# Performance work log

Hardware: AMD Instinct MI355X
Metric: run time of the kernel (lower is better)

Reference implementation:

```python
import jax, jax.numpy as jnp
import numpy as np

B, C_IN, V_IN = 16, 16, 16000
V1, V2 = 16384, 4096          # V2 = V1 // 4 (after first pool)
K1, K2 = 16, 16               # Chebyshev orders
F1, F2 = 32, 64               # conv output channels
FC1_F = 512
DEG = 16
EPS = 1e-5


def setup_inputs() -> dict:
    key = jax.random.key(0)
    ks = jax.random.split(key, 12)
    x = jax.random.normal(ks[0], (B, C_IN, V_IN), dtype=jnp.float32)
    perm_idx = jax.random.permutation(ks[1], V1).astype(jnp.int32)
    # sparse rescaled Laplacians in COO form (row, col, val)
    l1_rows = jnp.repeat(jnp.arange(V1, dtype=jnp.int32), DEG)
    l1_cols = jax.random.randint(ks[2], (V1 * DEG,), 0, V1, dtype=jnp.int32)
    l1_vals = jax.random.normal(ks[3], (V1 * DEG,), dtype=jnp.float32) / DEG
    l2_rows = jnp.repeat(jnp.arange(V2, dtype=jnp.int32), DEG)
    l2_cols = jax.random.randint(ks[4], (V2 * DEG,), 0, V2, dtype=jnp.int32)
    l2_vals = jax.random.normal(ks[5], (V2 * DEG,), dtype=jnp.float32) / DEG
    # Graph_Conv kernels: Linear(in_channels*K -> out_channels)
    s1 = np.sqrt(2.0 / (C_IN * K1 + F1)).astype(np.float32)
    w1 = jax.random.uniform(ks[6], (F1, C_IN * K1), jnp.float32, -s1, s1)
    b1 = jnp.zeros((F1,), jnp.float32)
    s2 = np.sqrt(2.0 / (F1 * K2 + F2)).astype(np.float32)
    w2 = jax.random.uniform(ks[7], (F2, F1 * K2), jnp.float32, -s2, s2)
    b2 = jnp.zeros((F2,), jnp.float32)
    fc_in = F2 * (V1 // 16)  # 65536
    s3 = np.sqrt(2.0 / (fc_in + FC1_F)).astype(np.float32)
    fc1_w = jax.random.uniform(ks[8], (FC1_F, fc_in), jnp.float32, -s3, s3)
    fc1_b = jnp.zeros((FC1_F,), jnp.float32)
    return dict(x=x, perm_idx=perm_idx,
                l1_rows=l1_rows, l1_cols=l1_cols, l1_vals=l1_vals,
                l2_rows=l2_rows, l2_cols=l2_cols, l2_vals=l2_vals,
                w1=w1, b1=b1, w2=w2, b2=b2, fc1_w=fc1_w, fc1_b=fc1_b)


def _spmm(rows, cols, vals, X, V):
    # sparse (V,V) @ dense (V,M) via gather + segment-sum
    return jax.ops.segment_sum(vals[:, None] * X[cols], rows, num_segments=V)


def _cheb_conv(x, rows, cols, vals, w, b, K):
    # x: (B, C, V) -> (B, Fout, V)
    Bn, C, V = x.shape
    x0 = x.transpose(2, 1, 0).reshape(V, C * Bn)
    xs = [x0]
    if K > 1:
        xs.append(_spmm(rows, cols, vals, x0, V))
    for _ in range(2, K):
        xs.append(2.0 * _spmm(rows, cols, vals, xs[-1], V) - xs[-2])
    xk = jnp.stack(xs, axis=0).reshape(K, V, C, Bn)    # (K, V, C, B)
    xk = xk.transpose(3, 1, 2, 0).reshape(Bn * V, C * K)
    y = xk @ w.T + b                                   # (B*V, Fout)
    return y.reshape(Bn, V, -1).transpose(0, 2, 1)     # (B, Fout, V)


def _pool4(x):
    Bn, C, V = x.shape
    return x.reshape(Bn, C, V // 4, 4).max(axis=-1)


def reference(x, perm_idx, l1_rows, l1_cols, l1_vals,
              l2_rows, l2_cols, l2_vals,
              w1, b1, w2, b2, fc1_w, fc1_b):
    # BatchNorm1d(affine=False), training-mode (batch) statistics
    mean = x.mean(axis=(0, 2), keepdims=True)
    var = x.var(axis=(0, 2), keepdims=True)
    x = (x - mean) * jax.lax.rsqrt(var + EPS)
    # Permute: zero-pad vertices to V1, then reorder
    Bn, C, V = x.shape
    x = jnp.pad(x, ((0, 0), (0, 0), (0, V1 - V)))[:, :, perm_idx]
    # conv1 -> relu -> pool4
    x = jax.nn.relu(_cheb_conv(x, l1_rows, l1_cols, l1_vals, w1, b1, K1))
    x = _pool4(x)
    # conv2 -> relu -> pool4
    x = jax.nn.relu(_cheb_conv(x, l2_rows, l2_cols, l2_vals, w2, b2, K2))
    x = _pool4(x)
    # flatten + fc1 (dropout is identity in eval mode)
    x = x.reshape(Bn, -1)
    return x @ fc1_w.T + fc1_b
```

## Files before the change

### kernel.cpp

```cpp
#include <hip/hip_runtime.h>

#define VIN  16000
#define V1q  16384
#define V2q  4096
#define Kq   16
#define F1q  32
#define F2q  64
#define FCIN 65536

typedef unsigned short u16;
typedef __attribute__((ext_vector_type(8))) short short8;
typedef __attribute__((ext_vector_type(4))) float f32x4;

__device__ __forceinline__ float bf2f(u16 v) { return __uint_as_float((unsigned)v << 16); }
__device__ __forceinline__ u16 f2bf(float f) {
    unsigned u = __float_as_uint(f);
    return (u16)((u + 0x7fffu + ((u >> 16) & 1u)) >> 16);
}

__global__ void bn_part(const float* __restrict__ x, float* __restrict__ part) {
    int c  = blockIdx.y;
    int bx = blockIdx.x;
    int b  = bx >> 2;
    int vc = bx & 3;
    const float* p = x + (size_t)(b * 16 + c) * VIN + vc * 4000;
    float s = 0.f, s2 = 0.f;
    for (int v = threadIdx.x; v < 4000; v += 256) {
        float val = p[v];
        s += val; s2 += val * val;
    }
    for (int o = 32; o; o >>= 1) { s += __shfl_down(s, o); s2 += __shfl_down(s2, o); }
    __shared__ float ls[4], ls2[4];
    int wid = threadIdx.x >> 6;
    if ((threadIdx.x & 63) == 0) { ls[wid] = s; ls2[wid] = s2; }
    __syncthreads();
    if (threadIdx.x == 0) {
        s = ls[0] + ls[1] + ls[2] + ls[3];
        s2 = ls2[0] + ls2[1] + ls2[2] + ls2[3];
        part[(c * 64 + bx) * 2]     = s;
        part[(c * 64 + bx) * 2 + 1] = s2;
    }
}

__global__ void bn_final(const float* __restrict__ part, float* __restrict__ mean_rstd) {
    int t = threadIdx.x;
    int c = t >> 4, j = t & 15;
    float s = 0.f, s2 = 0.f;
    for (int i = 0; i < 4; i++) {
        s  += part[(c * 64 + j * 4 + i) * 2];
        s2 += part[(c * 64 + j * 4 + i) * 2 + 1];
    }
    for (int o = 8; o; o >>= 1) { s += __shfl_down(s, o, 16); s2 += __shfl_down(s2, o, 16); }
    if (j == 0) {
        float m  = s / 256000.f;
        float var = s2 / 256000.f - m * m;
        mean_rstd[c]      = m;
        mean_rstd[16 + c] = rsqrtf(var + 1e-5f);
    }
}

__global__ void build_iperm(const int* __restrict__ perm, int* __restrict__ iperm) {
    int v = blockIdx.x * 256 + threadIdx.x;
    if (v < V1q) iperm[perm[v]] = v;
}

__global__ void norm_transpose_scatter(const float* __restrict__ x,
                                       const float* __restrict__ mean_rstd,
                                       const int* __restrict__ iperm,
                                       u16* __restrict__ X0) {
    __shared__ u16 tile[256][33];
    int u0 = blockIdx.x * 32;
    int t  = threadIdx.x;
    int jj = t & 31, half = t >> 5;
    for (int rr = 0; rr < 32; rr++) {
        int s = rr * 8 + half;
        int c = s & 15, b = s >> 4;
        float val = x[(size_t)s * VIN + u0 + jj];
        val = (val - mean_rstd[c]) * mean_rstd[16 + c];
        int d = ((c >> 3) << 7) | (b << 3) | (c & 7);
        tile[d][jj] = f2bf(val);
    }
    __syncthreads();
    for (int j = 0; j < 32; j++) {
        int tv = iperm[u0 + j];
        X0[(size_t)tv * 256 + t] = tile[t][j];
    }
}

__global__ void pack_w1(const float* __restrict__ w1, u16* __restrict__ B1p) {
    int i = blockIdx.x * 256 + threadIdx.x;
    int j = i & 7, l = (i >> 3) & 63, nf = (i >> 9) & 1, s = i >> 10;
    int q = l >> 4;
    int k = s * 2 + (q >> 1);
    int c = (q & 1) * 8 + j;
    int f = nf * 16 + (l & 15);
    B1p[i] = f2bf(w1[f * 256 + c * 16 + k]);
}
__global__ void pack_w2(const float* __restrict__ w2, u16* __restrict__ B2p) {
    int i = blockIdx.x * 256 + threadIdx.x;
    int j = i & 7, l = (i >> 3) & 63, nf = (i >> 9) & 3, k = i >> 11;
    int f1 = (l >> 4) * 8 + j;
    int f2 = nf * 16 + (l & 15);
    B2p[i] = f2bf(w2[f2 * 512 + f1 * 16 + k]);
}

template<int WLOG, int NRBLOG>
__global__ void spmm_cheb(const u16* __restrict__ prev, const u16* __restrict__ prev2,
                          u16* __restrict__ out,
                          const int* __restrict__ cols, const float* __restrict__ vals,
                          int nwg, float scale, int sub) {
    int bid = blockIdx.x;
    int q = nwg >> 3;
    int wid = (bid & 7) * q + (bid >> 3);
    int cb = wid >> NRBLOG;
    int r4 = wid & ((1 << NRBLOG) - 1);
    int lane = threadIdx.x & 63;
    int r = __builtin_amdgcn_readfirstlane(r4 * 4 + (threadIdx.x >> 6));
    int col = (cb << 6) + lane;
    const int4*   cp = (const int4*)(cols + r * 16);
    const float4* vp = (const float4*)(vals + r * 16);
    float acc = 0.f;
#pragma unroll
    for (int ii = 0; ii < 4; ii++) {
        int4   ci = cp[ii];
        float4 vi = vp[ii];
        const u16* p0 = prev + ((size_t)__builtin_amdgcn_readfirstlane(ci.x) << WLOG);
        const u16* p1 = prev + ((size_t)__builtin_amdgcn_readfirstlane(ci.y) << WLOG);
        const u16* p2 = prev + ((size_t)__builtin_amdgcn_readfirstlane(ci.z) << WLOG);
        const u16* p3 = prev + ((size_t)__builtin_amdgcn_readfirstlane(ci.w) << WLOG);
        acc += vi.x * bf2f(p0[col]);
        acc += vi.y * bf2f(p1[col]);
        acc += vi.z * bf2f(p2[col]);
        acc += vi.w * bf2f(p3[col]);
    }
    float o = scale * acc;
    if (sub) o -= bf2f(prev2[((size_t)r << WLOG) + col]);
    out[((size_t)r << WLOG) + col] = f2bf(o);
}

__launch_bounds__(256)
__global__ void gemm1_mfma(const u16* __restrict__ XS1, const u16* __restrict__ B1p,
                           const float* __restrict__ b1, u16* __restrict__ XS2_0) {
    __shared__ u16 As[2][4096];
    int t = threadIdx.x;
    int w = t >> 6, l = t & 63;
    int v0 = blockIdx.x * 8;
    int nf = w & 1, vq = w >> 1;

    f32x4 acc[4] = {};
    {
        const short8* s0 = (const short8*)(XS1 + (size_t)(0 * V1q + v0) * 256);
        const short8* s1 = (const short8*)(XS1 + (size_t)(1 * V1q + v0) * 256);
        short8* dst = (short8*)As[0];
        dst[t] = s0[t]; dst[256 + t] = s1[t];
    }
    __syncthreads();
    for (int s = 0; s < 8; s++) {
        int cur = s & 1;
        if (s < 7) {
            const short8* s0 = (const short8*)(XS1 + (size_t)((2 * s + 2) * V1q + v0) * 256);
            const short8* s1 = (const short8*)(XS1 + (size_t)((2 * s + 3) * V1q + v0) * 256);
            short8* dst = (short8*)As[cur ^ 1];
            dst[t] = s0[t]; dst[256 + t] = s1[t];
        }
        short8 bfrag = *(const short8*)(B1p + (((size_t)s * 2 + nf) * 64 + l) * 8);
        int abase = (l >> 5) * 2048 + (l & 31) * 8;
#pragma unroll
        for (int fm = 0; fm < 4; fm++) {
            int vl = vq * 4 + fm;
            short8 afrag = *(const short8*)&As[cur][abase + vl * 256];
            acc[fm] = __builtin_amdgcn_mfma_f32_16x16x32_bf16(afrag, bfrag, acc[fm], 0, 0, 0);
        }
        __syncthreads();
    }
    f32x4 m = acc[0];
#pragma unroll
    for (int fm = 1; fm < 4; fm++) {
#pragma unroll
        for (int i = 0; i < 4; i++) m[i] = fmaxf(m[i], acc[fm][i]);
    }
    int f1 = nf * 16 + (l & 15);
    float bias = b1[f1];
    int u_out = blockIdx.x * 2 + vq;
    u16* orow = XS2_0 + (size_t)u_out * 512;
    int colbase = ((f1 >> 3) << 7) | (f1 & 7);
#pragma unroll
    for (int reg = 0; reg < 4; reg++) {
        int b = (l >> 4) * 4 + reg;
        orow[colbase + b * 8] = f2bf(fmaxf(m[reg] + bias, 0.f));
    }
}

__launch_bounds__(256)
__global__ void gemm2_mfma(const u16* __restrict__ XS2, const u16* __restrict__ B2p,
                           const float* __restrict__ b2, float* __restrict__ P2f) {
    __shared__ u16 As[2][8192];
    __shared__ float ylds[4 * 16 * 66];
    int t = threadIdx.x;
    int w = t >> 6, l = t & 63;
    int u0 = blockIdx.x * 16;

    f32x4 acc[4][4] = {};
    {
        const short8* src = (const short8*)(XS2 + (size_t)(0 * V2q + u0) * 512);
        short8* dst = (short8*)As[0];
#pragma unroll
        for (int r = 0; r < 4; r++) dst[t * 4 + r] = src[t * 4 + r];
    }
    __syncthreads();
    for (int k = 0; k < 16; k++) {
        int cur = k & 1;
        if (k < 15) {
            const short8* src = (const short8*)(XS2 + (size_t)((k + 1) * V2q + u0) * 512);
            short8* dst = (short8*)As[cur ^ 1];
#pragma unroll
            for (int r = 0; r < 4; r++) dst[t * 4 + r] = src[t * 4 + r];
        }
        short8 bfrag[4];
#pragma unroll
        for (int nf = 0; nf < 4; nf++)
            bfrag[nf] = *(const short8*)(B2p + (((size_t)k * 4 + nf) * 64 + l) * 8);
#pragma unroll
        for (int fm = 0; fm < 4; fm++) {
            int ul = w * 4 + fm;
            short8 afrag = *(const short8*)&As[cur][ul * 512 + l * 8];
#pragma unroll
            for (int nf = 0; nf < 4; nf++)
                acc[fm][nf] = __builtin_amdgcn_mfma_f32_16x16x32_bf16(afrag, bfrag[nf], acc[fm][nf], 0, 0, 0);
        }
        __syncthreads();
    }
#pragma unroll
    for (int nf = 0; nf < 4; nf++) {
        int f2 = nf * 16 + (l & 15);
        float bias = b2[f2];
#pragma unroll
        for (int reg = 0; reg < 4; reg++) {
            int b = (l >> 4) * 4 + reg;
            float m = fmaxf(fmaxf(acc[0][nf][reg], acc[1][nf][reg]),
                            fmaxf(acc[2][nf][reg], acc[3][nf][reg]));
            ylds[(w * 16 + b) * 66 + f2] = fmaxf(m + bias, 0.f);
        }
    }
    __syncthreads();
    int ub = blockIdx.x * 4;
#pragma unroll
    for (int i = 0; i < 4; i++) {
        int p = t + i * 256;
        int b = p >> 6, f2 = p & 63;
        float4 v;
        v.x = ylds[(0 * 16 + b) * 66 + f2];
        v.y = ylds[(1 * 16 + b) * 66 + f2];
        v.z = ylds[(2 * 16 + b) * 66 + f2];
        v.w = ylds[(3 * 16 + b) * 66 + f2];
        *(float4*)&P2f[(size_t)(b * 64 + f2) * 1024 + ub] = v;
    }
}

__global__ void fc_init(const float* __restrict__ b, float* __restrict__ out) {
    int i = blockIdx.x * 256 + threadIdx.x;
    out[i] = b[i & 511];
}

__launch_bounds__(256)
__global__ void fc1k(const float* __restrict__ P2f, const float* __restrict__ W,
                     float* __restrict__ out) {
    __shared__ float red[4][64][17];
    int t = threadIdx.x;
    int w = t >> 6, l = t & 63;
    int o0 = blockIdx.x * 8 + w * 2;
    int k0 = blockIdx.y * 4096;
    const float* wr0 = W + (size_t)o0 * FCIN + k0;
    const float* wr1 = W + (size_t)(o0 + 1) * FCIN + k0;
    const float* pb  = P2f + k0;
    float acc0[16], acc1[16];
#pragma unroll
    for (int b = 0; b < 16; b++) { acc0[b] = 0.f; acc1[b] = 0.f; }
    for (int it = 0; it < 16; it++) {
        int kk = it * 256 + l * 4;
        float4 wa = *(const float4*)(wr0 + kk);
        float4 wb = *(const float4*)(wr1 + kk);
#pragma unroll
        for (int b = 0; b < 16; b++) {
            float4 p = *(const float4*)(pb + (size_t)b * FCIN + kk);
            acc0[b] += wa.x * p.x + wa.y * p.y + wa.z * p.z + wa.w * p.w;
            acc1[b] += wb.x * p.x + wb.y * p.y + wb.z * p.z + wb.w * p.w;
        }
    }
    int qq = l >> 4, bb = l & 15;
    __syncthreads();
#pragma unroll
    for (int b = 0; b < 16; b++) red[w][l][b] = acc0[b];
    __syncthreads();
    {
        float s = 0.f;
#pragma unroll
        for (int i = 0; i < 16; i++) s += red[w][qq * 16 + i][bb];
        s += __shfl_down(s, 16);
        s += __shfl_down(s, 32);
        if (l < 16) atomicAdd(&out[bb * 512 + o0], s);
    }
    __syncthreads();
#pragma unroll
    for (int b = 0; b < 16; b++) red[w][l][b] = acc1[b];
    __syncthreads();
    {
        float s = 0.f;
#pragma unroll
        for (int i = 0; i < 16; i++) s += red[w][qq * 16 + i][bb];
        s += __shfl_down(s, 16);
        s += __shfl_down(s, 32);
        if (l < 16) atomicAdd(&out[bb * 512 + o0 + 1], s);
    }
}

extern "C" void kernel_launch(void* const* d_in, const int* in_sizes, int n_in,
                              void* d_out, int out_size, void* d_ws, size_t ws_size,
                              hipStream_t stream) {
    const float* x       = (const float*)d_in[0];
    const int*   perm    = (const int*)d_in[1];
    const int*   l1_cols = (const int*)d_in[3];
    const float* l1_vals = (const float*)d_in[4];
    const int*   l2_cols = (const int*)d_in[6];
    const float* l2_vals = (const float*)d_in[7];
    const float* w1      = (const float*)d_in[8];
    const float* b1      = (const float*)d_in[9];
    const float* w2      = (const float*)d_in[10];
    const float* b2      = (const float*)d_in[11];
    const float* fcw     = (const float*)d_in[12];
    const float* fcb     = (const float*)d_in[13];
    float* out = (float*)d_out;

    char* wsb = (char*)d_ws;
    size_t off = 0;
    auto alloc = [&](size_t bytes) -> void* {
        void* p = wsb + off;
        off += (bytes + 255) & ~(size_t)255;
        return p;
    };
    float* mean_rstd = (float*)alloc(32 * 4);
    float* bnpart    = (float*)alloc(16 * 64 * 2 * 4);
    int*   iperm     = (int*)alloc((size_t)V1q * 4);
    u16*   B1p       = (u16*)alloc(8192 * 2);
    u16*   B2p       = (u16*)alloc(32768 * 2);
    u16*   XS1       = (u16*)alloc((size_t)Kq * V1q * 256 * 2);
    u16*   XS2       = (u16*)alloc((size_t)Kq * V2q * 512 * 2);
    float* P2f       = (float*)alloc((size_t)16 * FCIN * 4);
    (void)ws_size; (void)in_sizes; (void)n_in; (void)out_size;

    const size_t S1 = (size_t)V1q * 256;
    const size_t S2 = (size_t)V2q * 512;

    bn_part<<<dim3(64, 16), 256, 0, stream>>>(x, bnpart);
    bn_final<<<1, 256, 0, stream>>>(bnpart, mean_rstd);
    build_iperm<<<V1q / 256, 256, 0, stream>>>(perm, iperm);
    hipMemsetAsync(XS1, 0, S1 * 2, stream);
    norm_transpose_scatter<<<500, 256, 0, stream>>>(x, mean_rstd, iperm, XS1);
    pack_w1<<<32, 256, 0, stream>>>(w1, B1p);
    pack_w2<<<128, 256, 0, stream>>>(w2, B2p);

    spmm_cheb<8, 12><<<16384, 256, 0, stream>>>(XS1, XS1, XS1 + S1, l1_cols, l1_vals, 16384, 1.f, 0);
    for (int k = 2; k < Kq; k++)
        spmm_cheb<8, 12><<<16384, 256, 0, stream>>>(XS1 + (size_t)(k - 1) * S1, XS1 + (size_t)(k - 2) * S1,
                                                    XS1 + (size_t)k * S1, l1_cols, l1_vals, 16384, 2.f, 1);
    gemm1_mfma<<<V1q / 8, 256, 0, stream>>>(XS1, B1p, b1, XS2);

    spmm_cheb<9, 10><<<8192, 256, 0, stream>>>(XS2, XS2, XS2 + S2, l2_cols, l2_vals, 8192, 1.f, 0);
    for (int k = 2; k < Kq; k++)
        spmm_cheb<9, 10><<<8192, 256, 0, stream>>>(XS2 + (size_t)(k - 1) * S2, XS2 + (size_t)(k - 2) * S2,
                                                   XS2 + (size_t)k * S2, l2_cols, l2_vals, 8192, 2.f, 1);
    gemm2_mfma<<<V2q / 16, 256, 0, stream>>>(XS2, B2p, b2, P2f);

    fc_init<<<32, 256, 0, stream>>>(fcb, out);
    fc1k<<<dim3(64, 16), 256, 0, stream>>>(P2f, fcw, out);
}
```

Before: 506.8 us.

## Use bf16 MFMA for FC layer and nontemporal accesses in Chebyshev SpMM

Replaces the scalar-FMA fully connected kernel with an MFMA 16x16x32 bf16 kernel. Activations are first packed into fragment layout by a new pack_p kernel, and fp32 weights are converted to bf16 on the fly. The launch grid goes from 64x16 to 32x32 blocks, and a shared-memory reduction precedes the atomics. Separately, the SpMM's prev2 read and output write become nontemporal to reduce cache pollution. The FC change adds bf16 rounding of the weights and activations, which may affect accuracy.

```diff
diff --git a/kernel.cpp b/kernel.cpp
--- a/kernel.cpp
+++ b/kernel.cpp
@@ -102,6 +102,21 @@
     int f1 = (l >> 4) * 8 + j;
     int f2 = nf * 16 + (l & 15);
     B2p[i] = f2bf(w2[f2 * 512 + f1 * 16 + k]);
+}
+
+__global__ void pack_p(const float* __restrict__ P2f, u16* __restrict__ Pp) {
+    int i = blockIdx.x * 256 + threadIdx.x;
+    int l = i & 63, ks = i >> 6;
+    int b = l & 15, q = l >> 4;
+    const float* src = P2f + (size_t)b * FCIN + ks * 32 + q * 8;
+    float4 a0 = *(const float4*)(src);
+    float4 a1 = *(const float4*)(src + 4);
+    short8 v;
+    v[0] = (short)f2bf(a0.x); v[1] = (short)f2bf(a0.y);
+    v[2] = (short)f2bf(a0.z); v[3] = (short)f2bf(a0.w);
+    v[4] = (short)f2bf(a1.x); v[5] = (short)f2bf(a1.y);
+    v[6] = (short)f2bf(a1.z); v[7] = (short)f2bf(a1.w);
+    *(short8*)(Pp + (size_t)i * 8) = v;
 }
 
 template<int WLOG, int NRBLOG>
@@ -134,8 +149,8 @@
         acc += vi.w * bf2f(p3[col]);
     }
     float o = scale * acc;
-    if (sub) o -= bf2f(prev2[((size_t)r << WLOG) + col]);
-    out[((size_t)r << WLOG) + col] = f2bf(o);
+    if (sub) o -= bf2f(__builtin_nontemporal_load(prev2 + ((size_t)r << WLOG) + col));
+    __builtin_nontemporal_store(f2bf(o), out + ((size_t)r << WLOG) + col);
 }
 
 __launch_bounds__(256)
@@ -263,55 +278,34 @@
 }
 
 __launch_bounds__(256)
-__global__ void fc1k(const float* __restrict__ P2f, const float* __restrict__ W,
-                     float* __restrict__ out) {
-    __shared__ float red[4][64][17];
+__global__ void fc_mfma(const u16* __restrict__ Pp, const float* __restrict__ W,
+                        float* __restrict__ out) {
     int t = threadIdx.x;
     int w = t >> 6, l = t & 63;
-    int o0 = blockIdx.x * 8 + w * 2;
-    int k0 = blockIdx.y * 4096;
-    const float* wr0 = W + (size_t)o0 * FCIN + k0;
-    const float* wr1 = W + (size_t)(o0 + 1) * FCIN + k0;
-    const float* pb  = P2f + k0;
-    float acc0[16], acc1[16];
-#pragma unroll
-    for (int b = 0; b < 16; b++) { acc0[b] = 0.f; acc1[b] = 0.f; }
-    for (int it = 0; it < 16; it++) {
-        int kk = it * 256 + l * 4;
-        float4 wa = *(const float4*)(wr0 + kk);
-        float4 wb = *(const float4*)(wr1 + kk);
-#pragma unroll
-        for (int b = 0; b < 16; b++) {
-            float4 p = *(const float4*)(pb + (size_t)b * FCIN + kk);
-            acc0[b] += wa.x * p.x + wa.y * p.y + wa.z * p.z + wa.w * p.w;
-            acc1[b] += wb.x * p.x + wb.y * p.y + wb.z * p.z + wb.w * p.w;
-        }
-    }
-    int qq = l >> 4, bb = l & 15;
-    __syncthreads();
-#pragma unroll
-    for (int b = 0; b < 16; b++) red[w][l][b] = acc0[b];
-    __syncthreads();
-    {
-        float s = 0.f;
-#pragma unroll
-        for (int i = 0; i < 16; i++) s += red[w][qq * 16 + i][bb];
-        s += __shfl_down(s, 16);
-        s += __shfl_down(s, 32);
-        if (l < 16) atomicAdd(&out[bb * 512 + o0], s);
-    }
-    __syncthreads();
-#pragma unroll
-    for (int b = 0; b < 16; b++) red[w][l][b] = acc1[b];
-    __syncthreads();
-    {
-        float s = 0.f;
-#pragma unroll
-        for (int i = 0; i < 16; i++) s += red[w][qq * 16 + i][bb];
-        s += __shfl_down(s, 16);
-        s += __shfl_down(s, 32);
-        if (l < 16) atomicAdd(&out[bb * 512 + o0 + 1], s);
-    }
+    int n0 = blockIdx.x * 16;
+    int ks0 = blockIdx.y * 64 + w * 16;
+    int o = n0 + (l & 15);
+    const float* wp = W + (size_t)o * FCIN + (size_t)ks0 * 32 + (l >> 4) * 8;
+    const u16*   ap = Pp + ((size_t)ks0 * 64 + l) * 8;
+    f32x4 acc = {};
+    for (int s = 0; s < 16; s++) {
+        short8 afrag = *(const short8*)(ap + (size_t)s * 512);
+        float4 w0 = *(const float4*)(wp + s * 32);
+        float4 w1 = *(const float4*)(wp + s * 32 + 4);
+        short8 bfrag;
+        bfrag[0] = (short)f2bf(w0.x); bfrag[1] = (short)f2bf(w0.y);
+        bfrag[2] = (short)f2bf(w0.z); bfrag[3] = (short)f2bf(w0.w);
+        bfrag[4] = (short)f2bf(w1.x); bfrag[5] = (short)f2bf(w1.y);
+        bfrag[6] = (short)f2bf(w1.z); bfrag[7] = (short)f2bf(w1.w);
+        acc = __builtin_amdgcn_mfma_f32_16x16x32_bf16(afrag, bfrag, acc, 0, 0, 0);
+    }
+    __shared__ float red[4][256];
+#pragma unroll
+    for (int r = 0; r < 4; r++)
+        red[w][((l >> 4) * 4 + r) * 16 + (l & 15)] = acc[r];
+    __syncthreads();
+    float s = red[0][t] + red[1][t] + red[2][t] + red[3][t];
+    atomicAdd(&out[(t >> 4) * 512 + n0 + (t & 15)], s);
 }
 
 extern "C" void kernel_launch(void* const* d_in, const int* in_sizes, int n_in,
@@ -346,6 +340,7 @@
     u16*   XS1       = (u16*)alloc((size_t)Kq * V1q * 256 * 2);
     u16*   XS2       = (u16*)alloc((size_t)Kq * V2q * 512 * 2);
     float* P2f       = (float*)alloc((size_t)16 * FCIN * 4);
+    u16*   Pp        = (u16*)alloc((size_t)16 * FCIN * 2);
     (void)ws_size; (void)in_sizes; (void)n_in; (void)out_size;
 
     const size_t S1 = (size_t)V1q * 256;
@@ -371,6 +366,7 @@
                                                    XS2 + (size_t)k * S2, l2_cols, l2_vals, 8192, 2.f, 1);
     gemm2_mfma<<<V2q / 16, 256, 0, stream>>>(XS2, B2p, b2, P2f);
 
+    pack_p<<<512, 256, 0, stream>>>(P2f, Pp);
     fc_init<<<32, 256, 0, stream>>>(fcb, out);
-    fc1k<<<dim3(64, 16), 256, 0, stream>>>(P2f, fcw, out);
-}
+    fc_mfma<<<dim3(32, 32), 256, 0, stream>>>(Pp, fcw, out);
+}
```

After: 481.0 us. 5.1% less time.
